# Kernel tuning notes

Measured on AMD Instinct MI355X. Metric: run time of the kernel, lower is better.

Reference implementation:

```python
import jax, jax.numpy as jnp
import numpy as np

# geomloss SamplesLoss('sinkhorn', p=2, debias=True, reach=0.3, blur=0.01) constants
P = 2
BLUR = 0.01
REACH = 0.3
RHO = REACH ** P            # unbalanced KL strength rho = reach^p = 0.09
SCALING = 0.5               # geomloss default epsilon-scaling factor
DIAMETER = 1.0              # static diameter estimate (jit-friendly schedule)


def _eps_list():
    # geomloss epsilon_schedule(p, diameter, blur, scaling)
    eps = [DIAMETER ** P]
    eps += list(np.exp(np.arange(P * np.log(DIAMETER), P * np.log(BLUR), P * np.log(SCALING))))
    eps.append(BLUR ** P)
    return [float(e) for e in eps]


def _cost(x, y):
    # geomloss p=2 cost: |x - y|^2 / 2, shape [N, M]
    x2 = jnp.sum(x * x, axis=-1)[:, None]
    y2 = jnp.sum(y * y, axis=-1)[None, :]
    return 0.5 * (x2 + y2 - 2.0 * jnp.matmul(x, y.T))


def _softmin(eps, C, h):
    # h: log-weights (+ potential/eps), shape [M]; returns shape [N]
    return -eps * jax.nn.logsumexp(h[None, :] - C / eps, axis=1)


def _sinkhorn_divergence(x, y):
    N, M = x.shape[0], y.shape[0]
    a_log = jnp.full((N,), -np.log(N), dtype=x.dtype)   # uniform weights
    b_log = jnp.full((M,), -np.log(M), dtype=y.dtype)

    C_xy = _cost(x, y)
    C_yx = C_xy.T
    C_xx = _cost(x, x)
    C_yy = _cost(y, y)

    sg = jax.lax.stop_gradient
    Cxy_d, Cyx_d, Cxx_d, Cyy_d = sg(C_xy), sg(C_yx), sg(C_xx), sg(C_yy)

    eps_list = _eps_list()
    damp = lambda eps: 1.0 / (1.0 + eps / RHO)  # unbalanced dampening

    # init at largest blur (geomloss sinkhorn_loop)
    eps0 = eps_list[0]
    d0 = damp(eps0)
    g_ab = d0 * _softmin(eps0, Cyx_d, a_log)
    f_ba = d0 * _softmin(eps0, Cxy_d, b_log)
    f_aa = d0 * _softmin(eps0, Cxx_d, a_log)
    g_bb = d0 * _softmin(eps0, Cyy_d, b_log)

    # symmetric Sinkhorn updates with epsilon annealing (no grad, as in geomloss)
    for eps in eps_list:
        d = damp(eps)
        ft_ba = d * _softmin(eps, Cxy_d, b_log + g_ab / eps)
        gt_ab = d * _softmin(eps, Cyx_d, a_log + f_ba / eps)
        f_ba, g_ab = 0.5 * (f_ba + ft_ba), 0.5 * (g_ab + gt_ab)
        ft_aa = d * _softmin(eps, Cxx_d, a_log + f_aa / eps)
        gt_bb = d * _softmin(eps, Cyy_d, b_log + g_bb / eps)
        f_aa, g_bb = 0.5 * (f_aa + ft_aa), 0.5 * (g_bb + gt_bb)

    # last extrapolation at final blur, differentiable w.r.t. the cost
    eps = eps_list[-1]
    d = damp(eps)
    f_ba, g_ab = (d * _softmin(eps, C_xy, b_log + sg(g_ab) / eps),
                  d * _softmin(eps, C_yx, a_log + sg(f_ba) / eps))
    f_aa = d * _softmin(eps, C_xx, a_log + sg(f_aa) / eps)
    g_bb = d * _softmin(eps, C_yy, b_log + sg(g_bb) / eps)

    # unbalanced debiased Sinkhorn cost (geomloss sinkhorn_cost + UnbalancedWeight)
    a = jnp.exp(a_log)
    b = jnp.exp(b_log)
    w = RHO + eps / 2.0
    loss = w * (jnp.dot(a, jnp.exp(-f_aa / RHO) - jnp.exp(-f_ba / RHO))
                + jnp.dot(b, jnp.exp(-g_bb / RHO) - jnp.exp(-g_ab / RHO)))
    return loss


def setup_inputs() -> dict:
    key = jax.random.key(0)
    k1, k2, k3 = jax.random.split(key, 3)
    B, H, W = 512, 128, 128
    unnormed = jax.random.uniform(k1, (B, 1, H, W), dtype=jnp.float32)
    nd = jax.random.uniform(k2, (B, 1, H, W), dtype=jnp.float32)
    gt = jax.random.uniform(k3, (B, 1, H, W), dtype=jnp.float32)
    # normalized density maps sum to 1 per sample (as in DM-Count)
    nd = nd / jnp.sum(nd, axis=(1, 2, 3), keepdims=True)
    gt = gt / jnp.sum(gt, axis=(1, 2, 3), keepdims=True)
    return {"unnormed_density": unnormed, "normed_density": nd, "gt": gt}


def reference(unnormed_density, normed_density, gt):
    x = normed_density.reshape(normed_density.shape[0], -1)  # [B, HW]
    y = gt.reshape(gt.shape[0], -1)                          # [B, HW]
    loss = _sinkhorn_divergence(x, y)
    wd = 0
    ot_obj_values = jnp.zeros((1,), dtype=jnp.float32)
    return (loss, wd, ot_obj_values)
```

## Files before the change

kernel.cpp:

```cpp
#include <hip/hip_runtime.h>
#include <math.h>

#define HW 16384
#define NPTS 1024
#define LOG_N 6.2383246250395075
#define RHO_C 0.09
#define SCALE_F 16384.0f
#define INV_SCALE2 3.725290298461914e-09
#define NTILES 36

typedef _Float16 f16x8 __attribute__((ext_vector_type(8)));
typedef float f32x4 __attribute__((ext_vector_type(4)));

typedef __attribute__((address_space(1))) const void gvoid_t;
typedef __attribute__((address_space(3))) void svoid_t;

__device__ __forceinline__ void tri_map(int tt, int& ti, int& tj) {
  int a = 0, r = tt;
  while (r >= 8 - a) { r -= 8 - a; ++a; }
  ti = a; tj = a + r;
}

__global__ __launch_bounds__(256)
void convert_split_k(const float* __restrict__ nd, const float* __restrict__ gt,
                     _Float16* __restrict__ hi_t, _Float16* __restrict__ lo_t) {
  const int wt = blockIdx.x * 4 + (threadIdx.x >> 6);
  const int lane = threadIdx.x & 63;
  const int k64 = wt >> 6;
  const int rb = (wt & 63) << 4;
  const int g = lane & 7;
#pragma unroll
  for (int p = 0; p < 2; ++p) {
    const int row = rb + p * 8 + (lane >> 3);
    const float* __restrict__ src =
        (row < 512 ? nd + (size_t)row * HW : gt + (size_t)(row - 512) * HW) +
        k64 * 64 + g * 8;
    const float4 v0 = *(const float4*)(src);
    const float4 v1 = *(const float4*)(src + 4);
    const float x[8] = {v0.x, v0.y, v0.z, v0.w, v1.x, v1.y, v1.z, v1.w};
    f16x8 h, l;
#pragma unroll
    for (int j = 0; j < 8; ++j) {
      const float xs = x[j] * SCALE_F;
      const _Float16 hh = (_Float16)xs;
      h[j] = hh;
      l[j] = (_Float16)(xs - (float)hh);
    }
    const size_t o = ((size_t)k64 * 1024 + row) * 64 + (size_t)((g ^ (row & 7)) * 8);
    *(f16x8*)(hi_t + o) = h;
    *(f16x8*)(lo_t + o) = l;
  }
}

#define STAGE(BUF, KT)                                                          \
  {                                                                             \
    const size_t tb_ = (size_t)(KT) * 65536;                                    \
    const size_t ga_ = tb_ + (size_t)ti * 8192 + w * 1024 + lane * 8;           \
    const size_t gb_ = tb_ + (size_t)tj * 8192 + w * 1024 + lane * 8;           \
    _Float16* lb_ = lds + (BUF) * 32768 + w * 1024;                             \
    __builtin_amdgcn_global_load_lds((gvoid_t*)(hi_t + ga_), (svoid_t*)(lb_), 16, 0, 0);                   \
    __builtin_amdgcn_global_load_lds((gvoid_t*)(hi_t + ga_ + 512), (svoid_t*)(lb_ + 512), 16, 0, 0);       \
    __builtin_amdgcn_global_load_lds((gvoid_t*)(lo_t + ga_), (svoid_t*)(lb_ + 8192), 16, 0, 0);            \
    __builtin_amdgcn_global_load_lds((gvoid_t*)(lo_t + ga_ + 512), (svoid_t*)(lb_ + 8704), 16, 0, 0);      \
    __builtin_amdgcn_global_load_lds((gvoid_t*)(hi_t + gb_), (svoid_t*)(lb_ + 16384), 16, 0, 0);           \
    __builtin_amdgcn_global_load_lds((gvoid_t*)(hi_t + gb_ + 512), (svoid_t*)(lb_ + 16896), 16, 0, 0);     \
    __builtin_amdgcn_global_load_lds((gvoid_t*)(lo_t + gb_), (svoid_t*)(lb_ + 24576), 16, 0, 0);           \
    __builtin_amdgcn_global_load_lds((gvoid_t*)(lo_t + gb_ + 512), (svoid_t*)(lb_ + 25088), 16, 0, 0);     \
  }

__global__ __launch_bounds__(512, 2)
void gemm_mfma_k(const _Float16* __restrict__ hi_t, const _Float16* __restrict__ lo_t,
                 float* __restrict__ part, int ns) {
  extern __shared__ _Float16 lds[];

  const int nwg = NTILES * ns;
  const int b = blockIdx.x;
  const int k8 = b & 7, i8 = b >> 3;
  const int q8 = nwg >> 3, r8 = nwg & 7;
  const int start = (k8 < r8) ? k8 * (q8 + 1) : r8 * (q8 + 1) + (k8 - r8) * q8;
  const int lin = start + i8;
  const int c = lin / NTILES, tt = lin - c * NTILES;

  int ti, tj;
  tri_map(tt, ti, tj);
  const int q = 256 / ns, rm = 256 - q * ns;
  const int kt0 = c * q + (c < rm ? c : rm);
  const int nkt = q + (c < rm ? 1 : 0);
  const int t = threadIdx.x;
  const int lane = t & 63, w = t >> 6;
  const int wr = w >> 2, wc = w & 3;
  const int rlow = lane & 15, g0 = lane >> 4;
  const int sw = rlow & 7;

  f32x4 acc[4][2];
#pragma unroll
  for (int m = 0; m < 4; ++m)
#pragma unroll
    for (int n = 0; n < 2; ++n) acc[m][n] = (f32x4){0.f, 0.f, 0.f, 0.f};

  STAGE(0, kt0);
  __syncthreads();

  int cur = 0;
  for (int ks = 0; ks < nkt; ++ks) {
    if (ks + 1 < nkt) STAGE(cur ^ 1, kt0 + ks + 1);
    __builtin_amdgcn_sched_barrier(0);

    const _Float16* __restrict__ bb = lds + cur * 32768;
    f16x8 ah[2][4], al[2][4], bh[2][2], bl[2][2];
#pragma unroll
    for (int kk = 0; kk < 2; ++kk) {
      const int pe = ((kk * 4 + g0) ^ sw) * 8;
#pragma unroll
      for (int m = 0; m < 4; ++m) {
        const int ra = wr * 64 + m * 16 + rlow;
        ah[kk][m] = *(const f16x8*)(bb + ra * 64 + pe);
        al[kk][m] = *(const f16x8*)(bb + 8192 + ra * 64 + pe);
      }
#pragma unroll
      for (int n = 0; n < 2; ++n) {
        const int rb = wc * 32 + n * 16 + rlow;
        bh[kk][n] = *(const f16x8*)(bb + 16384 + rb * 64 + pe);
        bl[kk][n] = *(const f16x8*)(bb + 24576 + rb * 64 + pe);
      }
    }

    __builtin_amdgcn_s_setprio(1);
#pragma unroll
    for (int kk = 0; kk < 2; ++kk)
#pragma unroll
      for (int m = 0; m < 4; ++m)
#pragma unroll
        for (int n = 0; n < 2; ++n) {
          acc[m][n] = __builtin_amdgcn_mfma_f32_16x16x32_f16(ah[kk][m], bh[kk][n], acc[m][n], 0, 0, 0);
          acc[m][n] = __builtin_amdgcn_mfma_f32_16x16x32_f16(al[kk][m], bh[kk][n], acc[m][n], 0, 0, 0);
          acc[m][n] = __builtin_amdgcn_mfma_f32_16x16x32_f16(ah[kk][m], bl[kk][n], acc[m][n], 0, 0, 0);
        }
    __builtin_amdgcn_s_setprio(0);
    __syncthreads();
    cur ^= 1;
  }

  float* __restrict__ dst = part + ((size_t)c * NTILES + tt) * 16384;
  const int clb = wc * 32 + rlow;
  const int rlb = wr * 64 + g0 * 4;
#pragma unroll
  for (int m = 0; m < 4; ++m)
#pragma unroll
    for (int p = 0; p < 4; ++p) {
      const int rl = rlb + m * 16 + p;
#pragma unroll
      for (int n = 0; n < 2; ++n)
        dst[rl * 128 + clb + n * 16] = acc[m][n][p];
    }
}

__global__ __launch_bounds__(256)
void reduce_tiles_k(const float* __restrict__ part, float* __restrict__ G,
                    float* __restrict__ diag, int nsplit) {
  __shared__ float sl[8][129];
  const int blk = blockIdx.x;
  const int tt = blk >> 4, s = blk & 15;
  int ti, tj;
  tri_map(tt, ti, tj);
  const int t = threadIdx.x;
  const int base_in = tt * 16384 + s * 1024;

  float vals[4];
#pragma unroll
  for (int j = 0; j < 4; ++j) {
    const int idx = j * 256 + t;
    double a = 0.0;
    for (int c = 0; c < nsplit; ++c)
      a += (double)part[(size_t)c * (NTILES * 16384) + base_in + idx];
    vals[j] = (float)(a * INV_SCALE2);
  }
#pragma unroll
  for (int j = 0; j < 4; ++j) {
    const int idx = j * 256 + t;
    const int r = idx >> 7, cl = idx & 127;
    const int R = ti * 128 + s * 8 + r, C = tj * 128 + cl;
    G[(size_t)R * NPTS + C] = vals[j];
    if (R == C) diag[R] = vals[j];
    sl[r][cl] = vals[j];
  }
  if (ti == tj) return;
  __syncthreads();
#pragma unroll
  for (int j = 0; j < 4; ++j) {
    const int idx = j * 256 + t;
    const int r = idx & 7, cl = idx >> 3;
    G[(size_t)(tj * 128 + cl) * NPTS + ti * 128 + s * 8 + r] = sl[r][cl];
  }
}

__global__ __launch_bounds__(256)
void sinkhorn_phase_k(const float* __restrict__ G, const float* __restrict__ diag,
                      const double* __restrict__ src, double* __restrict__ dst,
                      double eps, double inv_eps, double damp, int use_pot,
                      int do_avg) {
  const int w = threadIdx.x >> 6, lane = threadIdx.x & 63;
  const int id = blockIdx.x * 4 + w;
  const int which = id >> 9, r = id & 511;
  int row_pt, col_base, pot_idx;
  if (which == 0)      { row_pt = r;       col_base = 512; pot_idx = 1; }
  else if (which == 1) { row_pt = 512 + r; col_base = 0;   pot_idx = 0; }
  else if (which == 2) { row_pt = r;       col_base = 0;   pot_idx = 2; }
  else                 { row_pt = 512 + r; col_base = 512; pot_idx = 3; }

  const double dr = (double)diag[row_pt];
  const double* __restrict__ pot = src + pot_idx * 512;
  const float* __restrict__ Grow = G + (size_t)row_pt * NPTS + col_base;
  const float* __restrict__ dcol = diag + col_base;

  double arg[8];
  double m = -1.0e300;
#pragma unroll
  for (int u = 0; u < 8; ++u) {
    const int j = lane + u * 64;
    const double C = 0.5 * (dr + (double)dcol[j]) - (double)Grow[j];
    const double p = use_pot ? pot[j] : 0.0;
    const double a = (p - C) * inv_eps - LOG_N;
    arg[u] = a;
    m = fmax(m, a);
  }
#pragma unroll
  for (int off = 32; off > 0; off >>= 1) m = fmax(m, __shfl_xor(m, off));
  double s = 0.0;
#pragma unroll
  for (int u = 0; u < 8; ++u) s += exp(arg[u] - m);
#pragma unroll
  for (int off = 32; off > 0; off >>= 1) s += __shfl_xor(s, off);
  if (lane == 0) {
    const double lse = m + log(s);
    const double val = -eps * lse * damp;
    dst[which * 512 + r] = do_avg ? 0.5 * (src[which * 512 + r] + val) : val;
  }
}

__global__ __launch_bounds__(256)
void loss_k(const double* __restrict__ pot, float* __restrict__ out, int out_size,
            double w) {
  const int t = threadIdx.x;
  double s = 0.0;
  for (int i = t; i < 512; i += 256) {
    s += (exp(-pot[1024 + i] / RHO_C) - exp(-pot[i] / RHO_C)) +
         (exp(-pot[1536 + i] / RHO_C) - exp(-pot[512 + i] / RHO_C));
  }
#pragma unroll
  for (int off = 32; off > 0; off >>= 1) s += __shfl_xor(s, off);
  __shared__ double wsum[4];
  if ((t & 63) == 0) wsum[t >> 6] = s;
  __syncthreads();
  if (t == 0) {
    out[0] = (float)(w * (wsum[0] + wsum[1] + wsum[2] + wsum[3]) * (1.0 / 512.0));
    for (int i = 1; i < out_size; ++i) out[i] = 0.f;
  }
}

extern "C" void kernel_launch(void* const* d_in, const int* in_sizes, int n_in,
                              void* d_out, int out_size, void* d_ws, size_t ws_size,
                              hipStream_t stream) {
  const float* nd = (const float*)d_in[1];
  const float* gt = (const float*)d_in[2];
  float* out = (float*)d_out;
  char* ws = (char*)d_ws;

  const size_t GM = (size_t)NPTS * NPTS;
  const size_t P16 = (size_t)NPTS * HW * 2;
  int nsplit = 7;
  while (nsplit > 1 &&
         2 * P16 + (size_t)nsplit * NTILES * 16384 * 4 + GM * 4 + 65536 > ws_size)
    nsplit >>= 1;

  _Float16* hi_t = (_Float16*)ws;
  _Float16* lo_t = (_Float16*)(ws + P16);
  float* part = (float*)(ws + 2 * P16);
  const size_t partsz = (size_t)nsplit * NTILES * 16384 * 4;
  float* G = (float*)(ws + 2 * P16 + partsz);
  float* diag = (float*)(ws + 2 * P16 + partsz + GM * 4);
  double* pots = (double*)(ws + 2 * P16 + partsz + GM * 4 + 8192);

  hipFuncSetAttribute((const void*)gemm_mfma_k,
                      hipFuncAttributeMaxDynamicSharedMemorySize, 131072);

  convert_split_k<<<4096, 256, 0, stream>>>(nd, gt, hi_t, lo_t);
  gemm_mfma_k<<<NTILES * nsplit, 512, 131072, stream>>>(hi_t, lo_t, part, nsplit);
  reduce_tiles_k<<<576, 256, 0, stream>>>(part, G, diag, nsplit);

  const double eps_list[9] = {1.0, 1.0, 0.25, 0.0625, 0.015625,
                              0.00390625, 0.0009765625, 0.000244140625, 1e-4};
  double* p0 = pots;
  double* p1 = pots + 2048;
  {
    const double eps = 1.0, d = 1.0 / (1.0 + eps / RHO_C);
    sinkhorn_phase_k<<<512, 256, 0, stream>>>(G, diag, p1, p0, eps, 1.0 / eps, d, 0, 0);
  }
  double* src = p0;
  double* dst = p1;
  for (int k = 0; k < 9; ++k) {
    const double eps = eps_list[k], d = 1.0 / (1.0 + eps / RHO_C);
    sinkhorn_phase_k<<<512, 256, 0, stream>>>(G, diag, src, dst, eps, 1.0 / eps, d, 1, 1);
    double* tmp = src; src = dst; dst = tmp;
  }
  {
    const double eps = 1e-4, d = 1.0 / (1.0 + eps / RHO_C);
    sinkhorn_phase_k<<<512, 256, 0, stream>>>(G, diag, src, dst, eps, 1.0 / eps, d, 1, 0);
    double* tmp = src; src = dst; dst = tmp;
  }
  loss_k<<<1, 256, 0, stream>>>(src, out, out_size, RHO_C + 1e-4 * 0.5);
}
```

Measured before the change: 140.9 us.

## Split K across wave halves with 64x64 wave tiles and skip diagonal B loads

Each of the 8 waves now computes a 64x64 sub-tile over half of the K=64 step, rather than a 64x32 sub-tile over the full step. This doubles per-wave register reuse of the A and B fragments and cuts LDS reads per MFMA. The two K halves are summed through LDS before the tile is written out. Diagonal tiles (ti==tj) reuse the A buffer as B and skip the redundant global loads for B. The trade-off is twice the accumulator registers per wave, which may hurt occupancy at launch_bounds(512,2), plus an extra LDS reduction and barrier at the end.

```diff
diff --git a/kernel.cpp b/kernel.cpp
--- a/kernel.cpp
+++ b/kernel.cpp
@@ -52,22 +52,6 @@
   }
 }
 
-#define STAGE(BUF, KT)                                                          \
-  {                                                                             \
-    const size_t tb_ = (size_t)(KT) * 65536;                                    \
-    const size_t ga_ = tb_ + (size_t)ti * 8192 + w * 1024 + lane * 8;           \
-    const size_t gb_ = tb_ + (size_t)tj * 8192 + w * 1024 + lane * 8;           \
-    _Float16* lb_ = lds + (BUF) * 32768 + w * 1024;                             \
-    __builtin_amdgcn_global_load_lds((gvoid_t*)(hi_t + ga_), (svoid_t*)(lb_), 16, 0, 0);                   \
-    __builtin_amdgcn_global_load_lds((gvoid_t*)(hi_t + ga_ + 512), (svoid_t*)(lb_ + 512), 16, 0, 0);       \
-    __builtin_amdgcn_global_load_lds((gvoid_t*)(lo_t + ga_), (svoid_t*)(lb_ + 8192), 16, 0, 0);            \
-    __builtin_amdgcn_global_load_lds((gvoid_t*)(lo_t + ga_ + 512), (svoid_t*)(lb_ + 8704), 16, 0, 0);      \
-    __builtin_amdgcn_global_load_lds((gvoid_t*)(hi_t + gb_), (svoid_t*)(lb_ + 16384), 16, 0, 0);           \
-    __builtin_amdgcn_global_load_lds((gvoid_t*)(hi_t + gb_ + 512), (svoid_t*)(lb_ + 16896), 16, 0, 0);     \
-    __builtin_amdgcn_global_load_lds((gvoid_t*)(lo_t + gb_), (svoid_t*)(lb_ + 24576), 16, 0, 0);           \
-    __builtin_amdgcn_global_load_lds((gvoid_t*)(lo_t + gb_ + 512), (svoid_t*)(lb_ + 25088), 16, 0, 0);     \
-  }
-
 __global__ __launch_bounds__(512, 2)
 void gemm_mfma_k(const _Float16* __restrict__ hi_t, const _Float16* __restrict__ lo_t,
                  float* __restrict__ part, int ns) {
@@ -83,20 +67,41 @@
 
   int ti, tj;
   tri_map(tt, ti, tj);
+  const bool dtile = (ti == tj);
   const int q = 256 / ns, rm = 256 - q * ns;
   const int kt0 = c * q + (c < rm ? c : rm);
   const int nkt = q + (c < rm ? 1 : 0);
   const int t = threadIdx.x;
   const int lane = t & 63, w = t >> 6;
-  const int wr = w >> 2, wc = w & 3;
+  const int pr = (w >> 1) & 1, pc = w & 1;
+  const int h = w >> 2;
   const int rlow = lane & 15, g0 = lane >> 4;
   const int sw = rlow & 7;
-
-  f32x4 acc[4][2];
+  const int boff = dtile ? 0 : 16384;
+
+  f32x4 acc[4][4];
 #pragma unroll
   for (int m = 0; m < 4; ++m)
 #pragma unroll
-    for (int n = 0; n < 2; ++n) acc[m][n] = (f32x4){0.f, 0.f, 0.f, 0.f};
+    for (int n = 0; n < 4; ++n) acc[m][n] = (f32x4){0.f, 0.f, 0.f, 0.f};
+
+#define STAGE(BUF, KT)                                                          \
+  {                                                                             \
+    const size_t tb_ = (size_t)(KT) * 65536;                                    \
+    const size_t ga_ = tb_ + (size_t)ti * 8192 + w * 1024 + lane * 8;           \
+    _Float16* lb_ = lds + (BUF) * 32768 + w * 1024;                             \
+    __builtin_amdgcn_global_load_lds((gvoid_t*)(hi_t + ga_), (svoid_t*)(lb_), 16, 0, 0);               \
+    __builtin_amdgcn_global_load_lds((gvoid_t*)(hi_t + ga_ + 512), (svoid_t*)(lb_ + 512), 16, 0, 0);   \
+    __builtin_amdgcn_global_load_lds((gvoid_t*)(lo_t + ga_), (svoid_t*)(lb_ + 8192), 16, 0, 0);        \
+    __builtin_amdgcn_global_load_lds((gvoid_t*)(lo_t + ga_ + 512), (svoid_t*)(lb_ + 8704), 16, 0, 0);  \
+    if (!dtile) {                                                               \
+      const size_t gb_ = tb_ + (size_t)tj * 8192 + w * 1024 + lane * 8;         \
+      __builtin_amdgcn_global_load_lds((gvoid_t*)(hi_t + gb_), (svoid_t*)(lb_ + 16384), 16, 0, 0);     \
+      __builtin_amdgcn_global_load_lds((gvoid_t*)(hi_t + gb_ + 512), (svoid_t*)(lb_ + 16896), 16, 0, 0);\
+      __builtin_amdgcn_global_load_lds((gvoid_t*)(lo_t + gb_), (svoid_t*)(lb_ + 24576), 16, 0, 0);     \
+      __builtin_amdgcn_global_load_lds((gvoid_t*)(lo_t + gb_ + 512), (svoid_t*)(lb_ + 25088), 16, 0, 0);\
+    }                                                                           \
+  }
 
   STAGE(0, kt0);
   __syncthreads();
@@ -107,52 +112,59 @@
     __builtin_amdgcn_sched_barrier(0);
 
     const _Float16* __restrict__ bb = lds + cur * 32768;
-    f16x8 ah[2][4], al[2][4], bh[2][2], bl[2][2];
-#pragma unroll
-    for (int kk = 0; kk < 2; ++kk) {
-      const int pe = ((kk * 4 + g0) ^ sw) * 8;
-#pragma unroll
-      for (int m = 0; m < 4; ++m) {
-        const int ra = wr * 64 + m * 16 + rlow;
-        ah[kk][m] = *(const f16x8*)(bb + ra * 64 + pe);
-        al[kk][m] = *(const f16x8*)(bb + 8192 + ra * 64 + pe);
+    const int pe = ((h * 4 + g0) ^ sw) * 8;
+    f16x8 ah[4], al[4], bh[4], bl[4];
+#pragma unroll
+    for (int m = 0; m < 4; ++m) {
+      const int ra = pr * 64 + m * 16 + rlow;
+      ah[m] = *(const f16x8*)(bb + ra * 64 + pe);
+      al[m] = *(const f16x8*)(bb + 8192 + ra * 64 + pe);
+      const int rb = pc * 64 + m * 16 + rlow;
+      bh[m] = *(const f16x8*)(bb + boff + rb * 64 + pe);
+      bl[m] = *(const f16x8*)(bb + boff + 8192 + rb * 64 + pe);
+    }
+
+    __builtin_amdgcn_s_setprio(1);
+#pragma unroll
+    for (int m = 0; m < 4; ++m)
+#pragma unroll
+      for (int n = 0; n < 4; ++n) {
+        acc[m][n] = __builtin_amdgcn_mfma_f32_16x16x32_f16(ah[m], bh[n], acc[m][n], 0, 0, 0);
+        acc[m][n] = __builtin_amdgcn_mfma_f32_16x16x32_f16(al[m], bh[n], acc[m][n], 0, 0, 0);
+        acc[m][n] = __builtin_amdgcn_mfma_f32_16x16x32_f16(ah[m], bl[n], acc[m][n], 0, 0, 0);
       }
-#pragma unroll
-      for (int n = 0; n < 2; ++n) {
-        const int rb = wc * 32 + n * 16 + rlow;
-        bh[kk][n] = *(const f16x8*)(bb + 16384 + rb * 64 + pe);
-        bl[kk][n] = *(const f16x8*)(bb + 24576 + rb * 64 + pe);
-      }
-    }
-
-    __builtin_amdgcn_s_setprio(1);
-#pragma unroll
-    for (int kk = 0; kk < 2; ++kk)
-#pragma unroll
-      for (int m = 0; m < 4; ++m)
-#pragma unroll
-        for (int n = 0; n < 2; ++n) {
-          acc[m][n] = __builtin_amdgcn_mfma_f32_16x16x32_f16(ah[kk][m], bh[kk][n], acc[m][n], 0, 0, 0);
-          acc[m][n] = __builtin_amdgcn_mfma_f32_16x16x32_f16(al[kk][m], bh[kk][n], acc[m][n], 0, 0, 0);
-          acc[m][n] = __builtin_amdgcn_mfma_f32_16x16x32_f16(ah[kk][m], bl[kk][n], acc[m][n], 0, 0, 0);
-        }
     __builtin_amdgcn_s_setprio(0);
     __syncthreads();
     cur ^= 1;
   }
 
-  float* __restrict__ dst = part + ((size_t)c * NTILES + tt) * 16384;
-  const int clb = wc * 32 + rlow;
-  const int rlb = wr * 64 + g0 * 4;
-#pragma unroll
-  for (int m = 0; m < 4; ++m)
-#pragma unroll
-    for (int p = 0; p < 4; ++p) {
-      const int rl = rlb + m * 16 + p;
-#pragma unroll
-      for (int n = 0; n < 2; ++n)
-        dst[rl * 128 + clb + n * 16] = acc[m][n][p];
-    }
+  float* red = (float*)lds;
+  if (h == 1) {
+    float* wb = red + (w & 3) * 4096;
+#pragma unroll
+    for (int m = 0; m < 4; ++m)
+#pragma unroll
+      for (int n = 0; n < 4; ++n)
+        *(f32x4*)(wb + (m * 4 + n) * 256 + lane * 4) = acc[m][n];
+  }
+  __syncthreads();
+  if (h == 0) {
+    float* wb = red + w * 4096;
+    float* __restrict__ dst = part + ((size_t)c * NTILES + tt) * 16384;
+    const int clb = pc * 64 + rlow;
+    const int rlb = pr * 64 + g0 * 4;
+#pragma unroll
+    for (int m = 0; m < 4; ++m)
+#pragma unroll
+      for (int n = 0; n < 4; ++n) {
+        const f32x4 o = *(const f32x4*)(wb + (m * 4 + n) * 256 + lane * 4);
+        const f32x4 s = acc[m][n] + o;
+#pragma unroll
+        for (int p = 0; p < 4; ++p)
+          dst[(rlb + m * 16 + p) * 128 + clb + n * 16] = s[p];
+      }
+  }
+#undef STAGE
 }
 
 __global__ __launch_bounds__(256)
```

After: 139.1 us. About the same (-1.3%).
